# Optimization experiments

Hardware: AMD Instinct MI355X
Metric: run time of the kernel (lower is better)

The kernel has to match this reference:

```python
import jax, jax.numpy as jnp
import numpy as np

D = 512       # input_dim
K = 8         # output_size (number of bilinear slices)
L = 64        # hash_length
Q = 4096      # number of query vectors
C = 4096      # number of class vectors


def setup_inputs() -> dict:
    key = jax.random.key(0)
    ks = jax.random.split(key, 8)
    class_vector = jax.random.normal(ks[0], (C, D), dtype=jnp.float32)
    query_vector = jax.random.normal(ks[1], (Q, D), dtype=jnp.float32)
    # xavier_normal over (D, D, K): std = sqrt(2 / (fan_in + fan_out))
    xav = float(np.sqrt(2.0 / (D + D)))
    M = jax.random.normal(ks[2], (D, D, K), dtype=jnp.float32) * xav
    # score_layer: Linear(K, 1)
    lim_s = 1.0 / np.sqrt(K)
    score_w = jax.random.uniform(ks[3], (K,), jnp.float32, -lim_s, lim_s)
    score_b = jax.random.uniform(ks[4], (1,), jnp.float32, -lim_s, lim_s)
    # hash_layer: Linear(D, L) + Tanh
    lim_h = 1.0 / np.sqrt(D)
    hash_w = jax.random.uniform(ks[5], (L, D), jnp.float32, -lim_h, lim_h)
    hash_b = jax.random.uniform(ks[6], (L,), jnp.float32, -lim_h, lim_h)
    return {
        "class_vector": class_vector,
        "query_vector": query_vector,
        "M": M,
        "score_w": score_w,
        "score_b": score_b,
        "hash_w": hash_w,
        "hash_b": hash_b,
    }


def reference(class_vector, query_vector, M, score_w, score_b, hash_w, hash_b):
    # Looped bilinear product fused into one einsum:
    # inter_k = Q @ (C @ M[:,:,k]).T  ->  [Q, C, K]
    bi = jnp.einsum('ci,ijk,qj->qck', class_vector, M, query_vector)
    act = jax.nn.relu(bi)
    # score_layer: Linear(K, 1) then squeeze -> [Q, C]
    other = jnp.einsum('qck,k->qc', act, score_w) + score_b[0]
    relation_scores = jax.nn.softmax(other, axis=1)       # softmax over class dim
    query_features = relation_scores @ class_vector + query_vector  # [Q, D]
    hash_codes = jnp.tanh(query_features @ hash_w.T + hash_b)       # [Q, L]
    return hash_codes
```

## Files before the change

### kernel.cpp

```cpp
#include <hip/hip_runtime.h>
#include <hip/hip_bf16.h>
#include <math.h>

#define D_ 512
#define K_ 8
#define L_ 64
#define Q_ 4096
#define C_ 4096
#define N_ (C_ * K_)

typedef short short8 __attribute__((ext_vector_type(8)));
typedef float f32x4 __attribute__((ext_vector_type(4)));

static __device__ __forceinline__ void split2(float v, unsigned short& h, unsigned short& l) {
    __hip_bfloat16 hh = __float2bfloat16(v);
    float r = v - __bfloat162float(hh);
    __hip_bfloat16 ll = __float2bfloat16(r);
    h = *reinterpret_cast<unsigned short*>(&hh);
    l = *reinterpret_cast<unsigned short*>(&ll);
}

#define ASYNC_COPY16(gp, lp)                                                        \
    __builtin_amdgcn_global_load_lds((const __attribute__((address_space(1))) void*)(gp), \
                                     (__attribute__((address_space(3))) void*)(lp), \
                                     16, 0, 0)

__global__ void transpose_M_split(const float* __restrict__ M,
                                  unsigned short* __restrict__ Mh,
                                  unsigned short* __restrict__ Ml) {
    int idx = blockIdx.x * blockDim.x + threadIdx.x;
    int i = idx & (D_ - 1);
    int n2 = idx >> 9;
    int j = n2 & (D_ - 1);
    int k = n2 >> 9;
    float v = M[((size_t)i * D_ + j) * K_ + k];
    split2(v, Mh[idx], Ml[idx]);
}

__global__ void split_f32(const float* __restrict__ x,
                          unsigned short* __restrict__ hi,
                          unsigned short* __restrict__ lo) {
    int i = blockIdx.x * blockDim.x + threadIdx.x;
    split2(x[i], hi[i], lo[i]);
}

__global__ void transpose_split_classT(const float* __restrict__ x,
                                       unsigned short* __restrict__ Th,
                                       unsigned short* __restrict__ Tl) {
    int idx = blockIdx.x * blockDim.x + threadIdx.x;
    int c = idx & (C_ - 1);
    int d = idx >> 12;
    float v = x[(size_t)c * D_ + d];
    split2(v, Th[idx], Tl[idx]);
}

#define OPS_ 8192
#define BUFS_ (4 * OPS_)

__device__ __forceinline__ void mfma_core8(
    const unsigned short* __restrict__ Agh, const unsigned short* __restrict__ Agl,
    const unsigned short* __restrict__ Bgh, const unsigned short* __restrict__ Bgl,
    const int lda, const int ldb, const int kd, const int m0, const int n0,
    unsigned short* Lds, f32x4 acc[8][4]) {
    const int tid = threadIdx.x;
    const int lane = tid & 63;
    const int wid = tid >> 6;
    const int fr = lane & 15;
    const int co = ((lane >> 4) ^ ((fr >> 1) & 3)) * 8;
    const int wm = (wid >> 2) * 128;
    const int wn = (wid & 3) * 64;
    const int nt = kd >> 5;
    const int aoff = (wm + fr) * 32 + co;
    const int boff = (wn + fr) * 32 + co;

#define STAGE8(k0_, buf_)                                                              \
    {                                                                                  \
        _Pragma("unroll")                                                              \
        for (int h_ = 0; h_ < 2; ++h_) {                                               \
            const int i2_ = h_ * 512 + tid;                                            \
            const int r_ = i2_ >> 2;                                                   \
            const int cg_ = (i2_ & 3) ^ ((r_ >> 1) & 3);                               \
            unsigned short* lp_ = Lds + (buf_) * BUFS_ + (h_ * 512 + (tid & ~63)) * 8; \
            const size_t ga_ = (size_t)(m0 + r_) * lda + (k0_) + cg_ * 8;              \
            const size_t gb_ = (size_t)(n0 + r_) * ldb + (k0_) + cg_ * 8;              \
            ASYNC_COPY16(Agh + ga_, lp_);                                              \
            ASYNC_COPY16(Agl + ga_, lp_ + OPS_);                                       \
            ASYNC_COPY16(Bgh + gb_, lp_ + 2 * OPS_);                                   \
            ASYNC_COPY16(Bgl + gb_, lp_ + 3 * OPS_);                                   \
        }                                                                              \
    }

#define QUAD(MH, NH)                                                                         \
    _Pragma("unroll")                                                                        \
    for (int i_ = 0; i_ < 4; ++i_) {                                                         \
        _Pragma("unroll")                                                                    \
        for (int j_ = 0; j_ < 2; ++j_) {                                                     \
            f32x4& a_ = acc[(MH) * 4 + i_][(NH) * 2 + j_];                                   \
            a_ = __builtin_amdgcn_mfma_f32_16x16x32_bf16(ah[i_], bhv[(NH) * 2 + j_], a_, 0, 0, 0); \
            a_ = __builtin_amdgcn_mfma_f32_16x16x32_bf16(ah[i_], blv[(NH) * 2 + j_], a_, 0, 0, 0); \
            a_ = __builtin_amdgcn_mfma_f32_16x16x32_bf16(al[i_], bhv[(NH) * 2 + j_], a_, 0, 0, 0); \
        }                                                                                    \
    }

    STAGE8(0, 0)
    STAGE8(32, 1)
    asm volatile("s_waitcnt vmcnt(8)" ::: "memory");
    __builtin_amdgcn_sched_barrier(0);
    __builtin_amdgcn_s_barrier();

#pragma unroll 2
    for (int t = 0; t < nt; ++t) {
        const int cur = t & 1;
        const unsigned short* Lc = Lds + cur * BUFS_;
        short8 ah[4], al[4], bhv[4], blv[4];

#pragma unroll
        for (int i = 0; i < 4; ++i) {
            ah[i] = *(const short8*)(Lc + aoff + i * 512);
            al[i] = *(const short8*)(Lc + OPS_ + aoff + i * 512);
        }
#pragma unroll
        for (int j = 0; j < 2; ++j) {
            bhv[j] = *(const short8*)(Lc + 2 * OPS_ + boff + j * 512);
            blv[j] = *(const short8*)(Lc + 3 * OPS_ + boff + j * 512);
        }
        __builtin_amdgcn_s_barrier();
        asm volatile("s_waitcnt lgkmcnt(0)" ::: "memory");
        __builtin_amdgcn_sched_barrier(0);
        __builtin_amdgcn_s_setprio(1);
        QUAD(0, 0)
        __builtin_amdgcn_s_setprio(0);
        __builtin_amdgcn_s_barrier();

#pragma unroll
        for (int j = 2; j < 4; ++j) {
            bhv[j] = *(const short8*)(Lc + 2 * OPS_ + boff + j * 512);
            blv[j] = *(const short8*)(Lc + 3 * OPS_ + boff + j * 512);
        }
        __builtin_amdgcn_s_barrier();
        asm volatile("s_waitcnt lgkmcnt(0)" ::: "memory");
        __builtin_amdgcn_sched_barrier(0);
        __builtin_amdgcn_s_setprio(1);
        QUAD(0, 1)
        __builtin_amdgcn_s_setprio(0);
        __builtin_amdgcn_s_barrier();

#pragma unroll
        for (int i = 0; i < 4; ++i) {
            ah[i] = *(const short8*)(Lc + aoff + 2048 + i * 512);
            al[i] = *(const short8*)(Lc + OPS_ + aoff + 2048 + i * 512);
        }
        __builtin_amdgcn_s_barrier();
        asm volatile("s_waitcnt lgkmcnt(0)" ::: "memory");
        __builtin_amdgcn_sched_barrier(0);
        __builtin_amdgcn_s_setprio(1);
        QUAD(1, 1)
        __builtin_amdgcn_s_setprio(0);
        __builtin_amdgcn_s_barrier();

        if (t + 2 < nt) STAGE8((t + 2) * 32, cur)
        __builtin_amdgcn_s_barrier();
        __builtin_amdgcn_s_setprio(1);
        QUAD(1, 0)
        __builtin_amdgcn_s_setprio(0);
        if (t + 2 < nt) {
            asm volatile("s_waitcnt vmcnt(8)" ::: "memory");
        } else if (t + 1 < nt) {
            asm volatile("s_waitcnt vmcnt(0)" ::: "memory");
        }
        __builtin_amdgcn_sched_barrier(0);
        __builtin_amdgcn_s_barrier();
    }
#undef STAGE8
#undef QUAD
}

__launch_bounds__(512, 2)
__global__ void gemm_P_mfma8(const unsigned short* __restrict__ Chh,
                             const unsigned short* __restrict__ Cll,
                             const unsigned short* __restrict__ Mh,
                             const unsigned short* __restrict__ Ml,
                             unsigned short* __restrict__ Ph,
                             unsigned short* __restrict__ Pl) {
    __shared__ __attribute__((aligned(16))) unsigned short Lds[2 * BUFS_];
    f32x4 acc[8][4] = {};
    const int n0 = blockIdx.x * 256;
    const int c0 = blockIdx.y * 256;
    mfma_core8(Chh, Cll, Mh, Ml, D_, D_, D_, c0, n0, Lds, acc);
    const int lane = threadIdx.x & 63;
    const int wid = threadIdx.x >> 6;
    const int fr = lane & 15, fq = lane >> 4;
    const int wm = (wid >> 2) * 128, wn = (wid & 3) * 64;
#pragma unroll
    for (int mi = 0; mi < 8; ++mi)
#pragma unroll
        for (int ni = 0; ni < 4; ++ni)
#pragma unroll
            for (int r = 0; r < 4; ++r) {
                int c = c0 + wm + mi * 16 + fq * 4 + r;
                int n2 = n0 + wn + ni * 16 + fr;
                size_t o = (size_t)c * (K_ * D_) + n2;
                split2(acc[mi][ni][r], Ph[o], Pl[o]);
            }
}

__launch_bounds__(512, 2)
__global__ void bilinear_mfma8(const unsigned short* __restrict__ Qh,
                               const unsigned short* __restrict__ Ql,
                               const unsigned short* __restrict__ Ph,
                               const unsigned short* __restrict__ Pl,
                               const float* __restrict__ sw,
                               const float* __restrict__ sb,
                               float* __restrict__ other) {
    __shared__ __attribute__((aligned(16))) unsigned short Lds[2 * BUFS_];
    f32x4 acc[8][4] = {};
    const int q0 = blockIdx.x * 256;
    const int n0 = blockIdx.y * 256;
    mfma_core8(Qh, Ql, Ph, Pl, D_, D_, D_, q0, n0, Lds, acc);
    const int lane = threadIdx.x & 63;
    const int wid = threadIdx.x >> 6;
    const int fr = lane & 15, fq = lane >> 4;
    const int wm = (wid >> 2) * 128, wn = (wid & 3) * 64;
    const float wk = sw[lane & 7];
    const float bias = sb[0];
#pragma unroll
    for (int mi = 0; mi < 8; ++mi)
#pragma unroll
        for (int ni = 0; ni < 4; ++ni)
#pragma unroll
            for (int r = 0; r < 4; ++r) {
                float v = wk * fmaxf(acc[mi][ni][r], 0.f);
                v += __shfl_xor(v, 1);
                v += __shfl_xor(v, 2);
                v += __shfl_xor(v, 4);
                if ((lane & 7) == 0) {
                    int q = q0 + wm + mi * 16 + fq * 4 + r;
                    int c = (n0 + wn + ni * 16 + fr) >> 3;
                    other[(size_t)q * C_ + c] = v + bias;
                }
            }
}

__launch_bounds__(512, 2)
__global__ void gemm_qf_mfma8(const unsigned short* __restrict__ Sh,
                              const unsigned short* __restrict__ Sl,
                              const unsigned short* __restrict__ Th,
                              const unsigned short* __restrict__ Tl,
                              float* __restrict__ qfp_base) {
    __shared__ __attribute__((aligned(16))) unsigned short Lds[2 * BUFS_];
    f32x4 acc[8][4] = {};
    const int n0 = blockIdx.x * 256;
    const int q0 = blockIdx.y * 256;
    const int zoff = blockIdx.z * (C_ / 8);
    float* qfp = qfp_base + (size_t)blockIdx.z * Q_ * D_;
    mfma_core8(Sh + zoff, Sl + zoff, Th + zoff, Tl + zoff,
               C_, C_, C_ / 8, q0, n0, Lds, acc);
    const int lane = threadIdx.x & 63;
    const int wid = threadIdx.x >> 6;
    const int fr = lane & 15, fq = lane >> 4;
    const int wm = (wid >> 2) * 128, wn = (wid & 3) * 64;
#pragma unroll
    for (int mi = 0; mi < 8; ++mi)
#pragma unroll
        for (int ni = 0; ni < 4; ++ni)
#pragma unroll
            for (int r = 0; r < 4; ++r) {
                int q = q0 + wm + mi * 16 + fq * 4 + r;
                int d = n0 + wn + ni * 16 + fr;
                qfp[(size_t)q * D_ + d] = acc[mi][ni][r];
            }
}

__launch_bounds__(256)
__global__ void softmax_split(const float* __restrict__ other,
                              unsigned short* __restrict__ Sh,
                              unsigned short* __restrict__ Sl) {
    const int q = blockIdx.x;
    const float* row = other + (size_t)q * C_;
    const int tid = threadIdx.x;
    __shared__ float red[4];
    float v[16];
    float m = -1e30f;
#pragma unroll
    for (int it = 0; it < 16; ++it) {
        v[it] = row[tid + it * 256];
        m = fmaxf(m, v[it]);
    }
#pragma unroll
    for (int off = 32; off; off >>= 1) m = fmaxf(m, __shfl_down(m, off));
    if ((tid & 63) == 0) red[tid >> 6] = m;
    __syncthreads();
    m = fmaxf(fmaxf(red[0], red[1]), fmaxf(red[2], red[3]));
    __syncthreads();
    float s = 0.f;
#pragma unroll
    for (int it = 0; it < 16; ++it) {
        v[it] = __expf(v[it] - m);
        s += v[it];
    }
#pragma unroll
    for (int off = 32; off; off >>= 1) s += __shfl_down(s, off);
    if ((tid & 63) == 0) red[tid >> 6] = s;
    __syncthreads();
    const float inv = 1.f / (red[0] + red[1] + red[2] + red[3]);
#pragma unroll
    for (int it = 0; it < 16; ++it) {
        size_t o = (size_t)q * C_ + tid + it * 256;
        split2(v[it] * inv, Sh[o], Sl[o]);
    }
}

__launch_bounds__(256)
__global__ void hash_kernel(const float* __restrict__ qfp_base,
                            const float* __restrict__ Qv,
                            const float* __restrict__ hw,
                            const float* __restrict__ hb,
                            float* __restrict__ out) {
    __shared__ float sqf[4 * D_];
    const int q0 = blockIdx.x * 4;
    const int tid = threadIdx.x;
    {
        const float4* sq = (const float4*)&Qv[(size_t)q0 * D_];
        float4* dst = (float4*)sqf;
#pragma unroll
        for (int it = 0; it < 2; ++it) {
            int i = tid + it * 256;
            float4 o = sq[i];
#pragma unroll
            for (int z = 0; z < 8; ++z) {
                const float4 a =
                    ((const float4*)&qfp_base[(size_t)z * Q_ * D_ + (size_t)q0 * D_])[i];
                o.x += a.x; o.y += a.y; o.z += a.z; o.w += a.w;
            }
            dst[i] = o;
        }
    }
    __syncthreads();
    const int l = tid % L_;
    const int qi = tid / L_;
    float s = hb[l];
    const float* wrow = &hw[(size_t)l * D_];
    const float* xrow = &sqf[qi * D_];
#pragma unroll 4
    for (int d = 0; d < D_; d += 4) {
        float4 w4 = *(const float4*)&wrow[d];
        float4 x4 = *(const float4*)&xrow[d];
        s += x4.x * w4.x + x4.y * w4.y + x4.z * w4.z + x4.w * w4.w;
    }
    out[(size_t)(q0 + qi) * L_ + l] = tanhf(s);
}

extern "C" void kernel_launch(void* const* d_in, const int* in_sizes, int n_in,
                              void* d_out, int out_size, void* d_ws, size_t ws_size,
                              hipStream_t stream) {
    const float* class_v = (const float*)d_in[0];
    const float* query_v = (const float*)d_in[1];
    const float* M       = (const float*)d_in[2];
    const float* score_w = (const float*)d_in[3];
    const float* score_b = (const float*)d_in[4];
    const float* hash_w  = (const float*)d_in[5];
    const float* hash_b  = (const float*)d_in[6];
    float* out = (float*)d_out;

    char* base = (char*)d_ws;
    unsigned short* Ph = (unsigned short*)base;
    unsigned short* Pl = (unsigned short*)(base + (size_t)33554432);
    char* oreg          = base + (size_t)67108864;
    float* other        = (float*)oreg;
    unsigned short* Mh  = (unsigned short*)oreg;
    unsigned short* Ml  = (unsigned short*)(oreg + (size_t)4194304);
    unsigned short* Chh = (unsigned short*)(oreg + (size_t)8388608);
    unsigned short* Cll = (unsigned short*)(oreg + (size_t)12582912);
    float* qfp          = (float*)oreg;
    char* scratch = base + (size_t)134217728;
    unsigned short* Qh = (unsigned short*)scratch;
    unsigned short* Ql = (unsigned short*)(scratch + (size_t)4194304);
    unsigned short* Th = (unsigned short*)scratch;
    unsigned short* Tl = (unsigned short*)(scratch + (size_t)4194304);
    unsigned short* Sh = Ph;
    unsigned short* Sl = Pl;

    transpose_M_split<<<(K_ * D_ * D_) / 256, 256, 0, stream>>>(M, Mh, Ml);
    split_f32<<<(C_ * D_) / 256, 256, 0, stream>>>(class_v, Chh, Cll);
    split_f32<<<(Q_ * D_) / 256, 256, 0, stream>>>(query_v, Qh, Ql);
    gemm_P_mfma8<<<dim3((K_ * D_) / 256, C_ / 256), 512, 0, stream>>>(Chh, Cll, Mh, Ml, Ph, Pl);
    bilinear_mfma8<<<dim3(Q_ / 256, N_ / 256), 512, 0, stream>>>(Qh, Ql, Ph, Pl,
                                                                 score_w, score_b, other);
    softmax_split<<<Q_, 256, 0, stream>>>(other, Sh, Sl);
    transpose_split_classT<<<(C_ * D_) / 256, 256, 0, stream>>>(class_v, Th, Tl);
    gemm_qf_mfma8<<<dim3(D_ / 256, Q_ / 256, 8), 512, 0, stream>>>(Sh, Sl, Th, Tl, qfp);
    hash_kernel<<<Q_ / 4, 256, 0, stream>>>(qfp, query_v, hash_w, hash_b, out);
}
```

Before: 724.4 us.

## Retile bilinear GEMM, add LDS-tiled transposes, and reorder MFMA chains

The dominant bilinear GEMM is replaced by a kernel with 128x128 tiles and 256 threads. It keeps B fragments in registers loaded straight from global memory and stages only A through LDS. A swizzled block-index mapping is added to improve L2 reuse. The naive strided transposes of M and class_vector are replaced by LDS-tiled transposes with coalesced reads and writes. The MFMA sequence in the shared core is reordered so consecutive instructions hit independent accumulators. The cost is smaller per-block reuse and direct global loads of the B fragments.

```diff
diff --git a/kernel.cpp b/kernel.cpp
--- a/kernel.cpp
+++ b/kernel.cpp
@@ -25,18 +25,6 @@
                                      (__attribute__((address_space(3))) void*)(lp), \
                                      16, 0, 0)
 
-__global__ void transpose_M_split(const float* __restrict__ M,
-                                  unsigned short* __restrict__ Mh,
-                                  unsigned short* __restrict__ Ml) {
-    int idx = blockIdx.x * blockDim.x + threadIdx.x;
-    int i = idx & (D_ - 1);
-    int n2 = idx >> 9;
-    int j = n2 & (D_ - 1);
-    int k = n2 >> 9;
-    float v = M[((size_t)i * D_ + j) * K_ + k];
-    split2(v, Mh[idx], Ml[idx]);
-}
-
 __global__ void split_f32(const float* __restrict__ x,
                           unsigned short* __restrict__ hi,
                           unsigned short* __restrict__ lo) {
@@ -44,14 +32,178 @@
     split2(x[i], hi[i], lo[i]);
 }
 
-__global__ void transpose_split_classT(const float* __restrict__ x,
+__global__ void transpose_M_split_tiled(const float* __restrict__ M,
+                                        unsigned short* __restrict__ Mh,
+                                        unsigned short* __restrict__ Ml) {
+    __shared__ float t[64 * 65];
+    const int t0 = blockIdx.x * 64;
+    const int i0 = blockIdx.y * 64;
+    const int tid = threadIdx.x;
+#pragma unroll
+    for (int it = 0; it < 16; ++it) {
+        int idx = tid + it * 256;
+        int ri = idx >> 6, tc = idx & 63;
+        t[tc * 65 + ri] = M[(size_t)(i0 + ri) * 4096 + t0 + tc];
+    }
+    __syncthreads();
+    const int j0 = t0 >> 3;
+#pragma unroll
+    for (int it = 0; it < 16; ++it) {
+        int odx = tid + it * 256;
+        int tl = odx >> 6, ic = odx & 63;
+        int n2 = (tl & 7) * 512 + j0 + (tl >> 3);
+        size_t o = (size_t)n2 * 512 + i0 + ic;
+        split2(t[tl * 65 + ic], Mh[o], Ml[o]);
+    }
+}
+
+__global__ void transpose_classT_tiled(const float* __restrict__ x,
                                        unsigned short* __restrict__ Th,
                                        unsigned short* __restrict__ Tl) {
-    int idx = blockIdx.x * blockDim.x + threadIdx.x;
-    int c = idx & (C_ - 1);
-    int d = idx >> 12;
-    float v = x[(size_t)c * D_ + d];
-    split2(v, Th[idx], Tl[idx]);
+    __shared__ float t[64 * 65];
+    const int c0 = blockIdx.x * 64;
+    const int d0 = blockIdx.y * 64;
+    const int tid = threadIdx.x;
+#pragma unroll
+    for (int it = 0; it < 16; ++it) {
+        int idx = tid + it * 256;
+        int rc = idx >> 6, dc = idx & 63;
+        t[dc * 65 + rc] = x[(size_t)(c0 + rc) * 512 + d0 + dc];
+    }
+    __syncthreads();
+#pragma unroll
+    for (int it = 0; it < 16; ++it) {
+        int odx = tid + it * 256;
+        int dr = odx >> 6, cc = odx & 63;
+        size_t o = (size_t)(d0 + dr) * 4096 + c0 + cc;
+        split2(t[dr * 65 + cc], Th[o], Tl[o]);
+    }
+}
+
+#define BM1 128
+#define BN1 128
+#define BNW1 32
+#define BKK1 32
+
+__device__ __forceinline__ void mfma_core(
+    const unsigned short* __restrict__ Agh, const unsigned short* __restrict__ Agl,
+    const unsigned short* __restrict__ Bgh, const unsigned short* __restrict__ Bgl,
+    int lda, int ldb, int kd, int m0, int n0,
+    unsigned short (*Ahb)[BM1 * BKK1], unsigned short (*Alb)[BM1 * BKK1],
+    f32x4 acc[8][2]) {
+    const int tid = threadIdx.x;
+    const int lane = tid & 63;
+    const int wid = tid >> 6;
+    const int fr = lane & 15;
+    const int fq = lane >> 4;
+    const int co = (fq ^ ((fr >> 1) & 3)) * 8;
+
+    const unsigned short* bh0 = Bgh + (size_t)(n0 + wid * BNW1 + fr) * ldb + fq * 8;
+    const unsigned short* bl0 = Bgl + (size_t)(n0 + wid * BNW1 + fr) * ldb + fq * 8;
+
+    short8 bh[2][2], bl[2][2];
+
+#pragma unroll
+    for (int h = 0; h < 2; ++h) {
+        const int i2 = h * 256 + tid;
+        const int r = i2 >> 2;
+        const int cg = (i2 & 3) ^ ((r >> 1) & 3);
+        const int ldsoff = (h * 256 + (tid & ~63)) * 8;
+        const size_t go = (size_t)(m0 + r) * lda + cg * 8;
+        ASYNC_COPY16(Agh + go, &Ahb[0][ldsoff]);
+        ASYNC_COPY16(Agl + go, &Alb[0][ldsoff]);
+    }
+    bh[0][0] = *(const short8*)(bh0);
+    bh[0][1] = *(const short8*)(bh0 + 16 * (size_t)ldb);
+    bl[0][0] = *(const short8*)(bl0);
+    bl[0][1] = *(const short8*)(bl0 + 16 * (size_t)ldb);
+    __syncthreads();
+
+    const int niter = kd / BKK1;
+#pragma unroll 2
+    for (int it = 0; it < niter; ++it) {
+        const int cur = it & 1, nxt = cur ^ 1;
+        if (it + 1 < niter) {
+            const int j0 = (it + 1) * BKK1;
+#pragma unroll
+            for (int h = 0; h < 2; ++h) {
+                const int i2 = h * 256 + tid;
+                const int r = i2 >> 2;
+                const int cg = (i2 & 3) ^ ((r >> 1) & 3);
+                const int ldsoff = (h * 256 + (tid & ~63)) * 8;
+                const size_t go = (size_t)(m0 + r) * lda + j0 + cg * 8;
+                ASYNC_COPY16(Agh + go, &Ahb[nxt][ldsoff]);
+                ASYNC_COPY16(Agl + go, &Alb[nxt][ldsoff]);
+            }
+            bh[nxt][0] = *(const short8*)(bh0 + j0);
+            bh[nxt][1] = *(const short8*)(bh0 + 16 * (size_t)ldb + j0);
+            bl[nxt][0] = *(const short8*)(bl0 + j0);
+            bl[nxt][1] = *(const short8*)(bl0 + 16 * (size_t)ldb + j0);
+        }
+#pragma unroll
+        for (int mi = 0; mi < 8; ++mi) {
+            const short8 ah = *(const short8*)&Ahb[cur][(mi * 16 + fr) * BKK1 + co];
+            const short8 al = *(const short8*)&Alb[cur][(mi * 16 + fr) * BKK1 + co];
+#pragma unroll
+            for (int ni = 0; ni < 2; ++ni)
+                acc[mi][ni] = __builtin_amdgcn_mfma_f32_16x16x32_bf16(ah, bh[cur][ni], acc[mi][ni], 0, 0, 0);
+#pragma unroll
+            for (int ni = 0; ni < 2; ++ni)
+                acc[mi][ni] = __builtin_amdgcn_mfma_f32_16x16x32_bf16(ah, bl[cur][ni], acc[mi][ni], 0, 0, 0);
+#pragma unroll
+            for (int ni = 0; ni < 2; ++ni)
+                acc[mi][ni] = __builtin_amdgcn_mfma_f32_16x16x32_bf16(al, bh[cur][ni], acc[mi][ni], 0, 0, 0);
+        }
+        __syncthreads();
+    }
+}
+
+__launch_bounds__(256, 4)
+__global__ void bilinear_mfma(const unsigned short* __restrict__ Qh,
+                              const unsigned short* __restrict__ Ql,
+                              const unsigned short* __restrict__ Ph,
+                              const unsigned short* __restrict__ Pl,
+                              const float* __restrict__ sw,
+                              const float* __restrict__ sb,
+                              float* __restrict__ other) {
+    __shared__ __attribute__((aligned(16))) unsigned short Ahb[2][BM1 * BKK1];
+    __shared__ __attribute__((aligned(16))) unsigned short Alb[2][BM1 * BKK1];
+    const int tid = threadIdx.x;
+    const int lane = tid & 63;
+    const int wid = tid >> 6;
+    const int fr = lane & 15;
+    const int fq = lane >> 4;
+    f32x4 acc[8][2] = {};
+
+    const int bid = blockIdx.x + (blockIdx.y << 5);
+    const int v = bid & 7;
+    const int c_ = bid >> 3;
+    const int g = c_ >> 8;
+    const int s = c_ & 255;
+    const int yb = v * 32 + g * 8 + (s >> 5);
+    const int xb = s & 31;
+    const int q0 = xb * BM1;
+    const int n0 = yb * BN1;
+
+    mfma_core(Qh, Ql, Ph, Pl, D_, D_, D_, q0, n0, Ahb, Alb, acc);
+    const float wk = sw[lane & 7];
+    const float bias = sb[0];
+#pragma unroll
+    for (int mi = 0; mi < 8; ++mi)
+#pragma unroll
+        for (int ni = 0; ni < 2; ++ni)
+#pragma unroll
+            for (int r = 0; r < 4; ++r) {
+                float v2 = wk * fmaxf(acc[mi][ni][r], 0.f);
+                v2 += __shfl_xor(v2, 1);
+                v2 += __shfl_xor(v2, 2);
+                v2 += __shfl_xor(v2, 4);
+                if ((lane & 7) == 0) {
+                    int q = q0 + mi * 16 + fq * 4 + r;
+                    int c = (n0 + wid * BNW1 + ni * 16 + fr) >> 3;
+                    other[(size_t)q * C_ + c] = v2 + bias;
+                }
+            }
 }
 
 #define OPS_ 8192
@@ -97,7 +249,21 @@
         for (int j_ = 0; j_ < 2; ++j_) {                                                     \
             f32x4& a_ = acc[(MH) * 4 + i_][(NH) * 2 + j_];                                   \
             a_ = __builtin_amdgcn_mfma_f32_16x16x32_bf16(ah[i_], bhv[(NH) * 2 + j_], a_, 0, 0, 0); \
+        }                                                                                    \
+    }                                                                                        \
+    _Pragma("unroll")                                                                        \
+    for (int i_ = 0; i_ < 4; ++i_) {                                                         \
+        _Pragma("unroll")                                                                    \
+        for (int j_ = 0; j_ < 2; ++j_) {                                                     \
+            f32x4& a_ = acc[(MH) * 4 + i_][(NH) * 2 + j_];                                   \
             a_ = __builtin_amdgcn_mfma_f32_16x16x32_bf16(ah[i_], blv[(NH) * 2 + j_], a_, 0, 0, 0); \
+        }                                                                                    \
+    }                                                                                        \
+    _Pragma("unroll")                                                                        \
+    for (int i_ = 0; i_ < 4; ++i_) {                                                         \
+        _Pragma("unroll")                                                                    \
+        for (int j_ = 0; j_ < 2; ++j_) {                                                     \
+            f32x4& a_ = acc[(MH) * 4 + i_][(NH) * 2 + j_];                                   \
             a_ = __builtin_amdgcn_mfma_f32_16x16x32_bf16(al[i_], bhv[(NH) * 2 + j_], a_, 0, 0, 0); \
         }                                                                                    \
     }
@@ -201,43 +367,6 @@
                 int n2 = n0 + wn + ni * 16 + fr;
                 size_t o = (size_t)c * (K_ * D_) + n2;
                 split2(acc[mi][ni][r], Ph[o], Pl[o]);
-            }
-}
-
-__launch_bounds__(512, 2)
-__global__ void bilinear_mfma8(const unsigned short* __restrict__ Qh,
-                               const unsigned short* __restrict__ Ql,
-                               const unsigned short* __restrict__ Ph,
-                               const unsigned short* __restrict__ Pl,
-                               const float* __restrict__ sw,
-                               const float* __restrict__ sb,
-                               float* __restrict__ other) {
-    __shared__ __attribute__((aligned(16))) unsigned short Lds[2 * BUFS_];
-    f32x4 acc[8][4] = {};
-    const int q0 = blockIdx.x * 256;
-    const int n0 = blockIdx.y * 256;
-    mfma_core8(Qh, Ql, Ph, Pl, D_, D_, D_, q0, n0, Lds, acc);
-    const int lane = threadIdx.x & 63;
-    const int wid = threadIdx.x >> 6;
-    const int fr = lane & 15, fq = lane >> 4;
-    const int wm = (wid >> 2) * 128, wn = (wid & 3) * 64;
-    const float wk = sw[lane & 7];
-    const float bias = sb[0];
-#pragma unroll
-    for (int mi = 0; mi < 8; ++mi)
-#pragma unroll
-        for (int ni = 0; ni < 4; ++ni)
-#pragma unroll
-            for (int r = 0; r < 4; ++r) {
-                float v = wk * fmaxf(acc[mi][ni][r], 0.f);
-                v += __shfl_xor(v, 1);
-                v += __shfl_xor(v, 2);
-                v += __shfl_xor(v, 4);
-                if ((lane & 7) == 0) {
-                    int q = q0 + wm + mi * 16 + fq * 4 + r;
-                    int c = (n0 + wn + ni * 16 + fr) >> 3;
-                    other[(size_t)q * C_ + c] = v + bias;
-                }
             }
 }
 
@@ -380,14 +509,14 @@
     unsigned short* Sh = Ph;
     unsigned short* Sl = Pl;
 
-    transpose_M_split<<<(K_ * D_ * D_) / 256, 256, 0, stream>>>(M, Mh, Ml);
+    transpose_M_split_tiled<<<dim3(64, 8), 256, 0, stream>>>(M, Mh, Ml);
     split_f32<<<(C_ * D_) / 256, 256, 0, stream>>>(class_v, Chh, Cll);
     split_f32<<<(Q_ * D_) / 256, 256, 0, stream>>>(query_v, Qh, Ql);
     gemm_P_mfma8<<<dim3((K_ * D_) / 256, C_ / 256), 512, 0, stream>>>(Chh, Cll, Mh, Ml, Ph, Pl);
-    bilinear_mfma8<<<dim3(Q_ / 256, N_ / 256), 512, 0, stream>>>(Qh, Ql, Ph, Pl,
-                                                                 score_w, score_b, other);
+    bilinear_mfma<<<dim3(Q_ / BM1, N_ / BN1), 256, 0, stream>>>(Qh, Ql, Ph, Pl,
+                                                                score_w, score_b, other);
     softmax_split<<<Q_, 256, 0, stream>>>(other, Sh, Sl);
-    transpose_split_classT<<<(C_ * D_) / 256, 256, 0, stream>>>(class_v, Th, Tl);
+    transpose_classT_tiled<<<dim3(64, 8), 256, 0, stream>>>(class_v, Th, Tl);
     gemm_qf_mfma8<<<dim3(D_ / 256, Q_ / 256, 8), 512, 0, stream>>>(Sh, Sl, Th, Tl, qfp);
     hash_kernel<<<Q_ / 4, 256, 0, stream>>>(qfp, query_v, hash_w, hash_b, out);
 }
```

New measurement: 734.9 us. Within noise of the previous version (+1.4%).
